# Kernel tuning notes

Measured on AMD Instinct MI355X. Metric: run time of the kernel, lower is better.

The kernel has to match this reference:

```python
import jax, jax.numpy as jnp
import numpy as np

N = 100000   # nodes
E = 500000   # edges
D = 128      # h_dim
R = 230      # relation types ('num_edges' in __init__)
B = 64       # num_bases
SI = D // B  # submat_in = 2
SO = D // B  # submat_out = 2
L = 2        # n_hidden_layers
RRELU_SLOPE = (1.0 / 8.0 + 1.0 / 3.0) / 2.0  # F.rrelu eval-mode negative slope


def setup_inputs() -> dict:
    key = jax.random.key(0)
    ks = jax.random.split(key, 9)
    ent_embeds = jax.random.normal(ks[0], (N, D), jnp.float32)
    rel_embeds = jax.random.normal(ks[1], (R, D), jnp.float32)
    # xavier_normal-ish scale for per-relation basis weights and self-loop weights
    weight = jax.random.normal(ks[2], (L, R, B * SI * SO), jnp.float32) * 0.1
    loop_weight = jax.random.normal(ks[3], (L, D, D), jnp.float32) * (2.0 / np.sqrt(2 * D))
    norm = jax.random.uniform(ks[4], (N, 1), jnp.float32)
    node_id = jax.random.randint(ks[5], (N,), 0, N)
    edge_type = jax.random.randint(ks[6], (E,), 0, R)
    src = jax.random.randint(ks[7], (E,), 0, N)
    dst = jax.random.randint(ks[8], (E,), 0, N)
    return dict(ent_embeds=ent_embeds, rel_embeds=rel_embeds, weight=weight,
                loop_weight=loop_weight, norm=norm, node_id=node_id,
                edge_type=edge_type, src=src, dst=dst)


def reference(ent_embeds, rel_embeds, weight, loop_weight, norm,
              node_id, edge_type, src, dst):
    # Aggregator.forward: h = ent_embeds[g.ndata['id']]
    h = ent_embeds[node_id]  # [N, D]
    # (rel_embeds are gathered into g.edata['h'] but unused by RGCNLayer)
    for l in range(L):
        # msg_func: per-edge basis-block weight gather + block-diag bmm
        w = weight[l][edge_type].reshape(E, B, SI, SO)   # [E, B, 2, 2]
        node = h[src].reshape(E, B, SI)                  # [E, B, 2]
        msg = jnp.einsum('ebi,ebio->ebo', node, w).reshape(E, D)
        # update_all scatter-sum + apply_func norm multiply
        agg = jax.ops.segment_sum(msg, dst, num_segments=N) * norm
        # self-loop message (dropout=0)
        agg = agg + h @ loop_weight[l]
        # F.rrelu in eval mode: leaky with slope (lower+upper)/2
        h = jnp.where(agg >= 0, agg, agg * RRELU_SLOPE)
    return h
```

## Files before the change

kernel.cpp:

```cpp
#include <hip/hip_runtime.h>
#include <hip/hip_bf16.h>

#define NN 100000
#define NE 500000
#define DD 128
#define RR 230
#define SLOPE 0.2291666666666666667f

#define EPMAX (NE + 7 * NN)
#define ZP (NN << 8)

typedef __attribute__((ext_vector_type(8))) short short8;
typedef __attribute__((ext_vector_type(4))) float f32x4;

__device__ __forceinline__ short f2bf(float f) {
    unsigned u = __float_as_uint(f);
    u += 0x7fffu + ((u >> 16) & 1u);
    return (short)(u >> 16);
}
__device__ __forceinline__ unsigned pkbf(float lo, float hi) {
    return (unsigned)(unsigned short)f2bf(lo) | ((unsigned)(unsigned short)f2bf(hi) << 16);
}

#if defined(__has_builtin)
#if __has_builtin(__builtin_amdgcn_fdot2_f32_bf16)
#define HAS_DOT2 1
#endif
#endif
__device__ __forceinline__ void dot2acc(float& acc, unsigned x, unsigned w) {
#ifdef HAS_DOT2
    typedef __attribute__((ext_vector_type(2))) __bf16 bf16x2;
    acc = __builtin_amdgcn_fdot2_f32_bf16(__builtin_bit_cast(bf16x2, x),
                                          __builtin_bit_cast(bf16x2, w), acc, false);
#else
    acc = fmaf(__uint_as_float(x << 16),        __uint_as_float(w << 16),
          fmaf(__uint_as_float(x & 0xFFFF0000u), __uint_as_float(w & 0xFFFF0000u), acc));
#endif
}

__global__ __launch_bounds__(256) void zero_k(int* __restrict__ cnt) {
    int i = blockIdx.x * 256 + threadIdx.x;
    if (i * 4 < NN) *(int4*)(cnt + i * 4) = make_int4(0, 0, 0, 0);
}

#define P1_WT_E   16
#define P1_WB_E   74
#define P1_FL_E   (74 + (EPMAX / 4 + 255) / 256)
#define P1_HB_E   (P1_FL_E + ((NN + 1) * 16 + 255) / 256)
#define P1_TOT    (P1_HB_E + (NE + 255) / 256)

__global__ __launch_bounds__(256) void p1_k(const float* __restrict__ lw,
                                            const float* __restrict__ weight,
                                            const float* __restrict__ ent,
                                            const int* __restrict__ nid,
                                            const int* __restrict__ dst,
                                            short* __restrict__ wt,
                                            unsigned* __restrict__ wb,
                                            unsigned short* __restrict__ hb,
                                            int* __restrict__ epack,
                                            int* __restrict__ cnt) {
    int bid = blockIdx.x;
    if (bid < P1_WT_E) {
        int gid = bid * 256 + threadIdx.x;
        if (gid >= 2 * DD * 16) return;
        int l   = gid >> 11;
        int rem = gid & 2047;
        int c   = rem >> 4;
        int u   = rem & 15;
        const float* wsrc = lw + l * DD * DD + c;
        short8 v;
        #pragma unroll
        for (int j = 0; j < 8; ++j) v[j] = f2bf(wsrc[(u * 8 + j) * DD]);
        *(short8*)(wt + (size_t)l * DD * DD + c * DD + ((u ^ (c & 7)) << 3)) = v;
    } else if (bid < P1_WB_E) {
        int gid = (bid - P1_WT_E) * 256 + threadIdx.x;
        if (gid >= 2 * RR * 32) return;
        int lt = gid >> 5;
        int hl = gid & 31;
        const float* wsrc = weight + (size_t)lt * 256 + hl * 8;
        float4 f0 = *(const float4*)wsrc;
        float4 f1 = *(const float4*)(wsrc + 4);
        uint4 v;
        v.x = pkbf(f0.x, f0.z);
        v.y = pkbf(f0.y, f0.w);
        v.z = pkbf(f1.x, f1.z);
        v.w = pkbf(f1.y, f1.w);
        *(uint4*)(wb + (size_t)lt * 128 + hl * 4) = v;
    } else if (bid < P1_FL_E) {
        int idx = (bid - P1_WB_E) * 256 + threadIdx.x;
        if (idx * 4 >= EPMAX) return;
        *(int4*)(epack + idx * 4) = make_int4(ZP, ZP, ZP, ZP);
    } else if (bid < P1_HB_E) {
        int gid = (bid - P1_FL_E) * 256 + threadIdx.x;
        if (gid >= (NN + 1) * 16) return;
        int n = gid >> 4;
        int u = gid & 15;
        short8 v = {0, 0, 0, 0, 0, 0, 0, 0};
        if (n < NN) {
            const float* srcp = ent + (size_t)nid[n] * DD + u * 8;
            float4 f0 = *(const float4*)srcp;
            float4 f1 = *(const float4*)(srcp + 4);
            v[0] = f2bf(f0.x); v[1] = f2bf(f0.y); v[2] = f2bf(f0.z); v[3] = f2bf(f0.w);
            v[4] = f2bf(f1.x); v[5] = f2bf(f1.y); v[6] = f2bf(f1.z); v[7] = f2bf(f1.w);
        }
        *(short8*)(hb + (size_t)n * DD + u * 8) = v;
    } else {
        int e = (bid - P1_HB_E) * 256 + threadIdx.x;
        if (e >= NE) return;
        atomicAdd(&cnt[dst[e]], 1);
    }
}

__global__ __launch_bounds__(256) void scan1_k(const int* __restrict__ cnt,
                                               int* __restrict__ off,
                                               int* __restrict__ bsum) {
    __shared__ int sh[256];
    int i = blockIdx.x * 256 + threadIdx.x;
    int v = (i < NN) ? ((cnt[i] + 7) & ~7) : 0;
    sh[threadIdx.x] = v;
    __syncthreads();
    for (int d = 1; d < 256; d <<= 1) {
        int t = (threadIdx.x >= d) ? sh[threadIdx.x - d] : 0;
        __syncthreads();
        sh[threadIdx.x] += t;
        __syncthreads();
    }
    if (i < NN) off[i] = sh[threadIdx.x] - v;
    if (threadIdx.x == 255) bsum[blockIdx.x] = sh[255];
}

__global__ __launch_bounds__(256) void scan23_k(int* __restrict__ off,
                                                const int* __restrict__ bsum,
                                                int* __restrict__ cursor,
                                                int nb) {
    __shared__ int sh[256];
    const int bid = blockIdx.x;
    const int tid = threadIdx.x;
    int s = 0;
    if (tid < bid) s = bsum[tid];
    if (tid + 256 < bid) s += bsum[tid + 256];
    sh[tid] = s;
    __syncthreads();
    #pragma unroll
    for (int d = 128; d > 0; d >>= 1) {
        if (tid < d) sh[tid] += sh[tid + d];
        __syncthreads();
    }
    const int S = sh[0];
    int i = bid * 256 + tid;
    if (i < NN) {
        int o = off[i] + S;
        off[i] = o;
        cursor[i] = o;
    }
    if (bid == nb - 1 && tid == 0) off[NN] = S + bsum[bid];
}

__global__ __launch_bounds__(256) void scat_k(const int* __restrict__ src,
                                              const int* __restrict__ et,
                                              const int* __restrict__ dst,
                                              int* __restrict__ cursor,
                                              int* __restrict__ epack) {
    int e = blockIdx.x * 256 + threadIdx.x;
    if (e >= NE) return;
    int pos = atomicAdd(&cursor[dst[e]], 1);
    epack[pos] = (src[e] << 8) | et[e];
}

__global__ __launch_bounds__(256) void agg_k(const unsigned short* __restrict__ hb,
                                             const int* __restrict__ off,
                                             const int* __restrict__ epack,
                                             const unsigned* __restrict__ wb,
                                             const float* __restrict__ norm,
                                             unsigned short* __restrict__ aggb) {
    int n    = (blockIdx.x * 256 + threadIdx.x) >> 6;
    int lane = threadIdx.x & 63;
    int hl   = lane & 31;
    int h2   = lane >> 5;
    if (n >= NN) return;
    int e0 = off[n];
    int m  = off[n + 1] - e0;
    float nv = norm[n];
    float a0 = 0.f, a1 = 0.f, a2 = 0.f, a3 = 0.f;
    const char* hbb = (const char*)hb + hl * 8;
    const char* wbb = (const char*)wb + hl * 16;
    const int*  ep  = epack + e0 + h2 * 4;

    for (int j = 0; j < m; j += 8) {
        uint4 pv = *(const uint4*)(ep + j);
        uint2 x0 = *(const uint2*)(hbb + (pv.x & 0xFFFFFF00u));
        uint2 x1 = *(const uint2*)(hbb + (pv.y & 0xFFFFFF00u));
        uint2 x2 = *(const uint2*)(hbb + (pv.z & 0xFFFFFF00u));
        uint2 x3 = *(const uint2*)(hbb + (pv.w & 0xFFFFFF00u));
        uint4 w0 = *(const uint4*)(wbb + ((pv.x & 255) << 9));
        uint4 w1 = *(const uint4*)(wbb + ((pv.y & 255) << 9));
        uint4 w2 = *(const uint4*)(wbb + ((pv.z & 255) << 9));
        uint4 w3 = *(const uint4*)(wbb + ((pv.w & 255) << 9));
        dot2acc(a0, x0.x, w0.x); dot2acc(a1, x0.x, w0.y);
        dot2acc(a2, x0.y, w0.z); dot2acc(a3, x0.y, w0.w);
        dot2acc(a0, x1.x, w1.x); dot2acc(a1, x1.x, w1.y);
        dot2acc(a2, x1.y, w1.z); dot2acc(a3, x1.y, w1.w);
        dot2acc(a0, x2.x, w2.x); dot2acc(a1, x2.x, w2.y);
        dot2acc(a2, x2.y, w2.z); dot2acc(a3, x2.y, w2.w);
        dot2acc(a0, x3.x, w3.x); dot2acc(a1, x3.x, w3.y);
        dot2acc(a2, x3.y, w3.z); dot2acc(a3, x3.y, w3.w);
    }
    a0 += __shfl_xor(a0, 32);
    a1 += __shfl_xor(a1, 32);
    a2 += __shfl_xor(a2, 32);
    a3 += __shfl_xor(a3, 32);
    if (h2 == 0) {
        uint2 pk;
        pk.x = pkbf(a0 * nv, a1 * nv);
        pk.y = pkbf(a2 * nv, a3 * nv);
        *(uint2*)(aggb + (size_t)n * DD + hl * 4) = pk;
    }
}

template<int WRITE_BF16>
__global__ __launch_bounds__(256, 2) void apply_k(const unsigned short* __restrict__ aggb,
                                                  const unsigned short* __restrict__ hb,
                                                  const short* __restrict__ Wt,
                                                  float* __restrict__ outf,
                                                  unsigned short* __restrict__ outb) {
    __shared__ short Ash[DD * DD];
    __shared__ short Wsh[DD * DD];

    const int tid = threadIdx.x;
    const long n0 = (long)blockIdx.x * 128;

    {
        const float4* wsrc = (const float4*)Wt;
        float4*       wdst = (float4*)Wsh;
        #pragma unroll
        for (int i = 0; i < 8; ++i) wdst[tid + i * 256] = wsrc[tid + i * 256];
    }
    {
        const int r  = tid >> 1;
        const int hf = tid & 1;
        long srow = n0 + r;
        if (srow >= NN) srow = NN - 1;
        const unsigned short* hrow = hb + (size_t)srow * DD + hf * 64;
        short* arow = Ash + r * DD;
        #pragma unroll
        for (int uu = 0; uu < 8; ++uu) {
            int u = hf * 8 + uu;
            short8 v = *(const short8*)(hrow + uu * 8);
            *(short8*)(arow + ((u ^ (r & 7)) << 3)) = v;
        }
    }
    __syncthreads();

    const int wv  = tid >> 6;
    const int wm  = wv >> 1;
    const int wn  = wv & 1;
    const int l16 = tid & 15;
    const int q   = (tid & 63) >> 4;

    f32x4 acc[4][4];
    #pragma unroll
    for (int mt = 0; mt < 4; ++mt)
        #pragma unroll
        for (int nt = 0; nt < 4; ++nt) acc[mt][nt] = (f32x4){0.f, 0.f, 0.f, 0.f};

    union Frag { uint2 u2[2]; short8 s8; };

    #pragma unroll
    for (int ks = 0; ks < 4; ++ks) {
        const int ua   = ks * 4 + (q >> 1);
        const int off8 = 4 * (q & 1);
        short8 af[4], bf[4];
        #pragma unroll
        for (int mt = 0; mt < 4; ++mt) {
            int r = wm * 64 + mt * 16 + l16;
            const short* base = Ash + r * DD;
            Frag fr;
            fr.u2[0] = *(const uint2*)(base + ((ua       ^ (r & 7)) << 3) + off8);
            fr.u2[1] = *(const uint2*)(base + (((ua + 2) ^ (r & 7)) << 3) + off8);
            af[mt] = fr.s8;
        }
        #pragma unroll
        for (int nt = 0; nt < 4; ++nt) {
            int c = wn * 64 + nt * 16 + l16;
            const short* base = Wsh + c * DD;
            Frag fr;
            fr.u2[0] = *(const uint2*)(base + ((ua       ^ (c & 7)) << 3) + off8);
            fr.u2[1] = *(const uint2*)(base + (((ua + 2) ^ (c & 7)) << 3) + off8);
            bf[nt] = fr.s8;
        }
        #pragma unroll
        for (int mt = 0; mt < 4; ++mt)
            #pragma unroll
            for (int nt = 0; nt < 4; ++nt)
                acc[mt][nt] = __builtin_amdgcn_mfma_f32_16x16x32_bf16(
                                  af[mt], bf[nt], acc[mt][nt], 0, 0, 0);
    }

    #pragma unroll
    for (int mt = 0; mt < 4; ++mt) {
        #pragma unroll
        for (int i = 0; i < 4; ++i) {
            long nrow = n0 + wm * 64 + mt * 16 + 4 * q + i;
            if (nrow < NN) {
                #pragma unroll
                for (int nt = 0; nt < 4; ++nt) {
                    int c = wn * 64 + nt * 16 + l16;
                    float g = __uint_as_float((unsigned)aggb[nrow * DD + c] << 16);
                    float v = g + acc[mt][nt][i];
                    v = (v >= 0.f) ? v : v * SLOPE;
                    if (WRITE_BF16) outb[nrow * DD + c] = (unsigned short)f2bf(v);
                    else            outf[nrow * DD + c] = v;
                }
            }
        }
    }
}

extern "C" void kernel_launch(void* const* d_in, const int* in_sizes, int n_in,
                              void* d_out, int out_size, void* d_ws, size_t ws_size,
                              hipStream_t stream) {
    const float* ent_embeds  = (const float*)d_in[0];
    const float* weight      = (const float*)d_in[2];
    const float* loop_weight = (const float*)d_in[3];
    const float* norm        = (const float*)d_in[4];
    const int*   node_id     = (const int*)d_in[5];
    const int*   edge_type   = (const int*)d_in[6];
    const int*   src         = (const int*)d_in[7];
    const int*   dst         = (const int*)d_in[8];
    float*       out         = (float*)d_out;

    unsigned short* aggb = (unsigned short*)d_ws;
    unsigned short* hb   = aggb + (size_t)NN * DD;
    int*   cnt    = (int*)(hb + (size_t)(NN + 1) * DD);
    int*   off    = cnt + NN;
    int*   cursor = off + NN + 1;
    int*   epack  = cursor + NN;
    int*   bsum   = epack + EPMAX;
    short* wt     = (short*)(bsum + 512);
    unsigned* wb  = (unsigned*)(wt + 2 * DD * DD);

    const int NB_E = (NE + 255) / 256;
    const int NB_N = (NN + 255) / 256;

    zero_k  <<<(NN / 4 + 255) / 256, 256, 0, stream>>>(cnt);
    p1_k    <<<P1_TOT, 256, 0, stream>>>(loop_weight, weight, ent_embeds, node_id, dst,
                                         wt, wb, hb, epack, cnt);
    scan1_k <<<NB_N, 256, 0, stream>>>(cnt, off, bsum);
    scan23_k<<<NB_N, 256, 0, stream>>>(off, bsum, cursor, NB_N);
    scat_k  <<<NB_E, 256, 0, stream>>>(src, edge_type, dst, cursor, epack);

    const int AGG_BLOCKS = (NN * 64) / 256;
    const int APL_BLOCKS = (NN + 127) / 128;

    agg_k     <<<AGG_BLOCKS, 256, 0, stream>>>(hb, off, epack, wb, norm, aggb);
    apply_k<1><<<APL_BLOCKS, 256, 0, stream>>>(aggb, hb, wt, nullptr, hb);

    agg_k     <<<AGG_BLOCKS, 256, 0, stream>>>(hb, off, epack, wb + (size_t)RR * 128,
                                               norm, aggb);
    apply_k<0><<<APL_BLOCKS, 256, 0, stream>>>(aggb, hb, wt + (size_t)DD * DD, out, nullptr);
}
```

Measured before the change: 197.3 us.

## Fuse edge aggregation and self-loop GEMM into one kernel per layer

Merges the per-node gather/aggregate kernel and the MFMA self-loop GEMM plus activation into a single 1024-thread kernel per layer. Each block handles 192 nodes and keeps the aggregated bf16 rows in shared memory, so the aggregate buffer no longer makes a global write-and-read round trip. The layer output now goes to a separate ping-pong buffer, because other blocks may still be reading rows of the input. The loop-weight matrix is no longer staged in LDS and its fragments are read straight from global memory. Occupancy is limited by the large blocks, and the GEMM tiles are smaller.

```diff
diff --git a/kernel.cpp b/kernel.cpp
--- a/kernel.cpp
+++ b/kernel.cpp
@@ -9,6 +9,9 @@
 
 #define EPMAX (NE + 7 * NN)
 #define ZP (NN << 8)
+
+#define NB   192
+#define ASTR 132
 
 typedef __attribute__((ext_vector_type(8))) short short8;
 typedef __attribute__((ext_vector_type(4))) float f32x4;
@@ -57,6 +60,7 @@
                                             short* __restrict__ wt,
                                             unsigned* __restrict__ wb,
                                             unsigned short* __restrict__ hb,
+                                            unsigned short* __restrict__ hb2,
                                             int* __restrict__ epack,
                                             int* __restrict__ cnt) {
     int bid = blockIdx.x;
@@ -102,6 +106,8 @@
             float4 f1 = *(const float4*)(srcp + 4);
             v[0] = f2bf(f0.x); v[1] = f2bf(f0.y); v[2] = f2bf(f0.z); v[3] = f2bf(f0.w);
             v[4] = f2bf(f1.x); v[5] = f2bf(f1.y); v[6] = f2bf(f1.z); v[7] = f2bf(f1.w);
+        } else {
+            *(short8*)(hb2 + (size_t)n * DD + u * 8) = v;
         }
         *(short8*)(hb + (size_t)n * DD + u * 8) = v;
     } else {
@@ -167,146 +173,123 @@
     epack[pos] = (src[e] << 8) | et[e];
 }
 
-__global__ __launch_bounds__(256) void agg_k(const unsigned short* __restrict__ hb,
-                                             const int* __restrict__ off,
-                                             const int* __restrict__ epack,
-                                             const unsigned* __restrict__ wb,
-                                             const float* __restrict__ norm,
-                                             unsigned short* __restrict__ aggb) {
-    int n    = (blockIdx.x * 256 + threadIdx.x) >> 6;
-    int lane = threadIdx.x & 63;
-    int hl   = lane & 31;
-    int h2   = lane >> 5;
-    if (n >= NN) return;
-    int e0 = off[n];
-    int m  = off[n + 1] - e0;
-    float nv = norm[n];
-    float a0 = 0.f, a1 = 0.f, a2 = 0.f, a3 = 0.f;
-    const char* hbb = (const char*)hb + hl * 8;
-    const char* wbb = (const char*)wb + hl * 16;
-    const int*  ep  = epack + e0 + h2 * 4;
-
-    for (int j = 0; j < m; j += 8) {
-        uint4 pv = *(const uint4*)(ep + j);
-        uint2 x0 = *(const uint2*)(hbb + (pv.x & 0xFFFFFF00u));
-        uint2 x1 = *(const uint2*)(hbb + (pv.y & 0xFFFFFF00u));
-        uint2 x2 = *(const uint2*)(hbb + (pv.z & 0xFFFFFF00u));
-        uint2 x3 = *(const uint2*)(hbb + (pv.w & 0xFFFFFF00u));
-        uint4 w0 = *(const uint4*)(wbb + ((pv.x & 255) << 9));
-        uint4 w1 = *(const uint4*)(wbb + ((pv.y & 255) << 9));
-        uint4 w2 = *(const uint4*)(wbb + ((pv.z & 255) << 9));
-        uint4 w3 = *(const uint4*)(wbb + ((pv.w & 255) << 9));
-        dot2acc(a0, x0.x, w0.x); dot2acc(a1, x0.x, w0.y);
-        dot2acc(a2, x0.y, w0.z); dot2acc(a3, x0.y, w0.w);
-        dot2acc(a0, x1.x, w1.x); dot2acc(a1, x1.x, w1.y);
-        dot2acc(a2, x1.y, w1.z); dot2acc(a3, x1.y, w1.w);
-        dot2acc(a0, x2.x, w2.x); dot2acc(a1, x2.x, w2.y);
-        dot2acc(a2, x2.y, w2.z); dot2acc(a3, x2.y, w2.w);
-        dot2acc(a0, x3.x, w3.x); dot2acc(a1, x3.x, w3.y);
-        dot2acc(a2, x3.y, w3.z); dot2acc(a3, x3.y, w3.w);
-    }
-    a0 += __shfl_xor(a0, 32);
-    a1 += __shfl_xor(a1, 32);
-    a2 += __shfl_xor(a2, 32);
-    a3 += __shfl_xor(a3, 32);
-    if (h2 == 0) {
-        uint2 pk;
-        pk.x = pkbf(a0 * nv, a1 * nv);
-        pk.y = pkbf(a2 * nv, a3 * nv);
-        *(uint2*)(aggb + (size_t)n * DD + hl * 4) = pk;
-    }
-}
-
 template<int WRITE_BF16>
-__global__ __launch_bounds__(256, 2) void apply_k(const unsigned short* __restrict__ aggb,
-                                                  const unsigned short* __restrict__ hb,
-                                                  const short* __restrict__ Wt,
-                                                  float* __restrict__ outf,
-                                                  unsigned short* __restrict__ outb) {
-    __shared__ short Ash[DD * DD];
-    __shared__ short Wsh[DD * DD];
-
-    const int tid = threadIdx.x;
-    const long n0 = (long)blockIdx.x * 128;
+__global__ __launch_bounds__(1024, 2) void fused_k(
+        const unsigned short* __restrict__ hsrc,
+        const int* __restrict__ off,
+        const int* __restrict__ epack,
+        const unsigned* __restrict__ wbl,
+        const short* __restrict__ wtl,
+        const float* __restrict__ norm,
+        float* __restrict__ outf,
+        unsigned short* __restrict__ outb) {
+    __shared__ unsigned short agg_sh[NB * ASTR];
+    __shared__ short Ash[64 * DD];
+
+    const int tid  = threadIdx.x;
+    const int n0   = blockIdx.x * NB;
+    const int lane = tid & 63;
+    const int w    = tid >> 6;
+    const int hl   = lane & 31;
+    const int h2   = lane >> 5;
 
     {
-        const float4* wsrc = (const float4*)Wt;
-        float4*       wdst = (float4*)Wsh;
+        const char* hbb = (const char*)hsrc + hl * 8;
+        const char* wbb = (const char*)wbl + hl * 16;
         #pragma unroll
-        for (int i = 0; i < 8; ++i) wdst[tid + i * 256] = wsrc[tid + i * 256];
-    }
-    {
-        const int r  = tid >> 1;
-        const int hf = tid & 1;
-        long srow = n0 + r;
-        if (srow >= NN) srow = NN - 1;
-        const unsigned short* hrow = hb + (size_t)srow * DD + hf * 64;
-        short* arow = Ash + r * DD;
+        for (int i = 0; i < NB / 16; ++i) {
+            int n = n0 + w + 16 * i;
+            if (n >= NN) break;
+            int e0 = off[n];
+            int m  = off[n + 1] - e0;
+            float nv = norm[n];
+            float a0 = 0.f, a1 = 0.f, a2 = 0.f, a3 = 0.f;
+            const int* ep = epack + e0 + h2 * 4;
+            for (int j = 0; j < m; j += 8) {
+                uint4 pv = *(const uint4*)(ep + j);
+                uint2 x0 = *(const uint2*)(hbb + (pv.x & 0xFFFFFF00u));
+                uint2 x1 = *(const uint2*)(hbb + (pv.y & 0xFFFFFF00u));
+                uint2 x2 = *(const uint2*)(hbb + (pv.z & 0xFFFFFF00u));
+                uint2 x3 = *(const uint2*)(hbb + (pv.w & 0xFFFFFF00u));
+                uint4 w0 = *(const uint4*)(wbb + ((pv.x & 255) << 9));
+                uint4 w1 = *(const uint4*)(wbb + ((pv.y & 255) << 9));
+                uint4 w2 = *(const uint4*)(wbb + ((pv.z & 255) << 9));
+                uint4 w3 = *(const uint4*)(wbb + ((pv.w & 255) << 9));
+                dot2acc(a0, x0.x, w0.x); dot2acc(a1, x0.x, w0.y);
+                dot2acc(a2, x0.y, w0.z); dot2acc(a3, x0.y, w0.w);
+                dot2acc(a0, x1.x, w1.x); dot2acc(a1, x1.x, w1.y);
+                dot2acc(a2, x1.y, w1.z); dot2acc(a3, x1.y, w1.w);
+                dot2acc(a0, x2.x, w2.x); dot2acc(a1, x2.x, w2.y);
+                dot2acc(a2, x2.y, w2.z); dot2acc(a3, x2.y, w2.w);
+                dot2acc(a0, x3.x, w3.x); dot2acc(a1, x3.x, w3.y);
+                dot2acc(a2, x3.y, w3.z); dot2acc(a3, x3.y, w3.w);
+            }
+            a0 += __shfl_xor(a0, 32);
+            a1 += __shfl_xor(a1, 32);
+            a2 += __shfl_xor(a2, 32);
+            a3 += __shfl_xor(a3, 32);
+            if (h2 == 0) {
+                int nl = w + 16 * i;
+                uint2 pk;
+                pk.x = pkbf(a0 * nv, a1 * nv);
+                pk.y = pkbf(a2 * nv, a3 * nv);
+                *(uint2*)(&agg_sh[nl * ASTR + hl * 4]) = pk;
+            }
+        }
+    }
+
+    const int wm  = w >> 2;
+    const int wn  = w & 3;
+    const int l16 = tid & 15;
+    const int q   = lane >> 4;
+    union Frag { uint2 u2[2]; short8 s8; };
+
+    for (int sub = 0; sub < NB / 64; ++sub) {
+        __syncthreads();
+        {
+            int r = tid >> 4;
+            int u = tid & 15;
+            long srow = n0 + sub * 64 + r;
+            if (srow >= NN) srow = NN - 1;
+            short8 v = *(const short8*)(hsrc + (size_t)srow * DD + u * 8);
+            *(short8*)(Ash + r * DD + ((u ^ (r & 7)) << 3)) = v;
+        }
+        __syncthreads();
+
+        f32x4 acc[2];
+        acc[0] = (f32x4){0.f, 0.f, 0.f, 0.f};
+        acc[1] = (f32x4){0.f, 0.f, 0.f, 0.f};
+        const int ar = wm * 16 + l16;
+        const short* abase = Ash + ar * DD;
         #pragma unroll
-        for (int uu = 0; uu < 8; ++uu) {
-            int u = hf * 8 + uu;
-            short8 v = *(const short8*)(hrow + uu * 8);
-            *(short8*)(arow + ((u ^ (r & 7)) << 3)) = v;
-        }
-    }
-    __syncthreads();
-
-    const int wv  = tid >> 6;
-    const int wm  = wv >> 1;
-    const int wn  = wv & 1;
-    const int l16 = tid & 15;
-    const int q   = (tid & 63) >> 4;
-
-    f32x4 acc[4][4];
-    #pragma unroll
-    for (int mt = 0; mt < 4; ++mt)
+        for (int ks = 0; ks < 4; ++ks) {
+            const int ua   = ks * 4 + (q >> 1);
+            const int off8 = 4 * (q & 1);
+            Frag fa;
+            fa.u2[0] = *(const uint2*)(abase + ((ua       ^ (ar & 7)) << 3) + off8);
+            fa.u2[1] = *(const uint2*)(abase + (((ua + 2) ^ (ar & 7)) << 3) + off8);
+            #pragma unroll
+            for (int nt = 0; nt < 2; ++nt) {
+                int c = wn * 32 + nt * 16 + l16;
+                const short* bbase = wtl + (size_t)c * DD;
+                Frag fb;
+                fb.u2[0] = *(const uint2*)(bbase + ((ua       ^ (c & 7)) << 3) + off8);
+                fb.u2[1] = *(const uint2*)(bbase + (((ua + 2) ^ (c & 7)) << 3) + off8);
+                acc[nt] = __builtin_amdgcn_mfma_f32_16x16x32_bf16(fa.s8, fb.s8,
+                                                                  acc[nt], 0, 0, 0);
+            }
+        }
+
         #pragma unroll
-        for (int nt = 0; nt < 4; ++nt) acc[mt][nt] = (f32x4){0.f, 0.f, 0.f, 0.f};
-
-    union Frag { uint2 u2[2]; short8 s8; };
-
-    #pragma unroll
-    for (int ks = 0; ks < 4; ++ks) {
-        const int ua   = ks * 4 + (q >> 1);
-        const int off8 = 4 * (q & 1);
-        short8 af[4], bf[4];
-        #pragma unroll
-        for (int mt = 0; mt < 4; ++mt) {
-            int r = wm * 64 + mt * 16 + l16;
-            const short* base = Ash + r * DD;
-            Frag fr;
-            fr.u2[0] = *(const uint2*)(base + ((ua       ^ (r & 7)) << 3) + off8);
-            fr.u2[1] = *(const uint2*)(base + (((ua + 2) ^ (r & 7)) << 3) + off8);
-            af[mt] = fr.s8;
-        }
-        #pragma unroll
-        for (int nt = 0; nt < 4; ++nt) {
-            int c = wn * 64 + nt * 16 + l16;
-            const short* base = Wsh + c * DD;
-            Frag fr;
-            fr.u2[0] = *(const uint2*)(base + ((ua       ^ (c & 7)) << 3) + off8);
-            fr.u2[1] = *(const uint2*)(base + (((ua + 2) ^ (c & 7)) << 3) + off8);
-            bf[nt] = fr.s8;
-        }
-        #pragma unroll
-        for (int mt = 0; mt < 4; ++mt)
+        for (int nt = 0; nt < 2; ++nt) {
+            int c = wn * 32 + nt * 16 + l16;
             #pragma unroll
-            for (int nt = 0; nt < 4; ++nt)
-                acc[mt][nt] = __builtin_amdgcn_mfma_f32_16x16x32_bf16(
-                                  af[mt], bf[nt], acc[mt][nt], 0, 0, 0);
-    }
-
-    #pragma unroll
-    for (int mt = 0; mt < 4; ++mt) {
-        #pragma unroll
-        for (int i = 0; i < 4; ++i) {
-            long nrow = n0 + wm * 64 + mt * 16 + 4 * q + i;
-            if (nrow < NN) {
-                #pragma unroll
-                for (int nt = 0; nt < 4; ++nt) {
-                    int c = wn * 64 + nt * 16 + l16;
-                    float g = __uint_as_float((unsigned)aggb[nrow * DD + c] << 16);
-                    float v = g + acc[mt][nt][i];
+            for (int i = 0; i < 4; ++i) {
+                int rl = sub * 64 + wm * 16 + 4 * q + i;
+                long nrow = (long)n0 + rl;
+                if (nrow < NN) {
+                    float g = __uint_as_float((unsigned)agg_sh[rl * ASTR + c] << 16);
+                    float v = g + acc[nt][i];
                     v = (v >= 0.f) ? v : v * SLOPE;
                     if (WRITE_BF16) outb[nrow * DD + c] = (unsigned short)f2bf(v);
                     else            outf[nrow * DD + c] = v;
@@ -329,9 +312,9 @@
     const int*   dst         = (const int*)d_in[8];
     float*       out         = (float*)d_out;
 
-    unsigned short* aggb = (unsigned short*)d_ws;
-    unsigned short* hb   = aggb + (size_t)NN * DD;
-    int*   cnt    = (int*)(hb + (size_t)(NN + 1) * DD);
+    unsigned short* hb  = (unsigned short*)d_ws;
+    unsigned short* hb2 = hb + (size_t)(NN + 1) * DD;
+    int*   cnt    = (int*)(hb2 + (size_t)(NN + 1) * DD);
     int*   off    = cnt + NN;
     int*   cursor = off + NN + 1;
     int*   epack  = cursor + NN;
@@ -344,18 +327,17 @@
 
     zero_k  <<<(NN / 4 + 255) / 256, 256, 0, stream>>>(cnt);
     p1_k    <<<P1_TOT, 256, 0, stream>>>(loop_weight, weight, ent_embeds, node_id, dst,
-                                         wt, wb, hb, epack, cnt);
+                                         wt, wb, hb, hb2, epack, cnt);
     scan1_k <<<NB_N, 256, 0, stream>>>(cnt, off, bsum);
     scan23_k<<<NB_N, 256, 0, stream>>>(off, bsum, cursor, NB_N);
     scat_k  <<<NB_E, 256, 0, stream>>>(src, edge_type, dst, cursor, epack);
 
-    const int AGG_BLOCKS = (NN * 64) / 256;
-    const int APL_BLOCKS = (NN + 127) / 128;
-
-    agg_k     <<<AGG_BLOCKS, 256, 0, stream>>>(hb, off, epack, wb, norm, aggb);
-    apply_k<1><<<APL_BLOCKS, 256, 0, stream>>>(aggb, hb, wt, nullptr, hb);
-
-    agg_k     <<<AGG_BLOCKS, 256, 0, stream>>>(hb, off, epack, wb + (size_t)RR * 128,
-                                               norm, aggb);
-    apply_k<0><<<APL_BLOCKS, 256, 0, stream>>>(aggb, hb, wt + (size_t)DD * DD, out, nullptr);
-}
+    const int FUSED_BLOCKS = (NN + NB - 1) / NB;
+
+    fused_k<1><<<FUSED_BLOCKS, 1024, 0, stream>>>(hb, off, epack, wb, wt,
+                                                  norm, nullptr, hb2);
+    fused_k<0><<<FUSED_BLOCKS, 1024, 0, stream>>>(hb2, off, epack,
+                                                  wb + (size_t)RR * 128,
+                                                  wt + (size_t)DD * DD,
+                                                  norm, out, nullptr);
+}
```

Result: slower. 243.6 us (+23.5%).
